# Performance work log

Measured on AMD Instinct MI355X. Metric: run time of the kernel, lower is better.

Reference implementation:

```python
import jax, jax.numpy as jnp
import numpy as np

N = 100000
E = 1_600_000
IN_X, OUT_X = 128, 128
IN_E, OUT_E = 32, 128


def setup_inputs() -> dict:
    key = jax.random.key(0)
    k1, k2, k3, k4, k5, k6, k7 = jax.random.split(key, 7)
    x = jax.random.normal(k1, (N, IN_X), dtype=jnp.float32)
    edge_index = jax.random.randint(k2, (2, E), 0, N, dtype=jnp.int64)
    edge_attr = jax.random.normal(k3, (E, IN_E), dtype=jnp.float32)
    Wx = jax.random.normal(k4, (IN_X, OUT_X), dtype=jnp.float32) * (1.0 / np.sqrt(IN_X))
    bx = jax.random.normal(k5, (OUT_X,), dtype=jnp.float32) * 0.01
    We = jax.random.normal(k6, (IN_E, OUT_E), dtype=jnp.float32) * (1.0 / np.sqrt(IN_E))
    be = jax.random.normal(k7, (OUT_E,), dtype=jnp.float32) * 0.01
    return {"x": x, "edge_index": edge_index, "edge_attr": edge_attr,
            "Wx": Wx, "bx": bx, "We": We, "be": be}


def reference(x, edge_index, edge_attr, Wx, bx, We, be):
    # torch: to_dense() -> [N, N, in_e]; sum over dim=1 == scatter-add of
    # edge_attr into rows indexed by the source node edge_index[0].
    agg = jax.ops.segment_sum(edge_attr, edge_index[0], num_segments=x.shape[0])  # [N, in_e]
    hx = x @ Wx + bx          # [N, out_x]
    he = agg @ We + be        # [N, out_e]
    return jnp.concatenate((hx, he), axis=1)  # [N, out_x + out_e]
```

## Files before the change

kernel.cpp:

```cpp
#include <hip/hip_runtime.h>


#define BSHIFT    7
#define BSIZE     128
#define NBMAX     1024
#define SEG_CAP   3584
#define POOL_SZ   3648
#define CHUNK_A   8192
#define SPILL_CAP 65536

typedef short bf16x8 __attribute__((ext_vector_type(8)));
typedef float f32x4  __attribute__((ext_vector_type(4)));

__device__ __forceinline__ unsigned short f2bf(float f) {
    union { float f; unsigned u; } c; c.f = f;
    unsigned u = c.u;
    u += 0x7FFF + ((u >> 16) & 1);
    return (unsigned short)(u >> 16);
}

__global__ __launch_bounds__(512) void binA_kernel(
    const int* __restrict__ src, int E, int nb,
    unsigned* __restrict__ segs, int* __restrict__ gcnt,
    int2* __restrict__ spill, int* __restrict__ spillcnt)
{
    __shared__ unsigned pool[CHUNK_A];
    __shared__ int hist[NBMAX];
    __shared__ int offs[NBMAX];
    __shared__ int lcur[NBMAX];
    __shared__ int gbase[NBMAX];
    __shared__ int gallow[NBMAX];
    __shared__ int wsum[8];

    int tid = threadIdx.x;
    int base = blockIdx.x * CHUNK_A;

    for (int i = tid; i < NBMAX; i += 512) hist[i] = 0;
    __syncthreads();

    for (int i = tid; i < CHUNK_A; i += 512) {
        int e = base + i;
        if (e < E) atomicAdd(&hist[src[e] >> BSHIFT], 1);
    }
    __syncthreads();

    {
        int t2 = tid * 2;
        int c0 = hist[t2], c1 = hist[t2 + 1];
        int s = c0 + c1;
        int lane = tid & 63, wid = tid >> 6;
        int ws = s;
        #pragma unroll
        for (int d = 1; d < 64; d <<= 1) {
            int t = __shfl_up(ws, d);
            if (lane >= d) ws += t;
        }
        if (lane == 63) wsum[wid] = ws;
        __syncthreads();
        int woff = 0;
        #pragma unroll
        for (int w = 0; w < 8; ++w) if (w < wid) woff += wsum[w];
        int ex = woff + ws - s;
        offs[t2] = ex;          lcur[t2] = ex;
        offs[t2 + 1] = ex + c0; lcur[t2 + 1] = ex + c0;
    }
    __syncthreads();

    {
        int t2 = tid * 2;
        #pragma unroll
        for (int u = 0; u < 2; ++u) {
            int b = t2 + u;
            if (b < nb) {
                int cnt = hist[b];
                int b0 = cnt ? atomicAdd(&gcnt[b], cnt) : 0;
                gbase[b] = b0;
                int allow = SEG_CAP - b0;
                if (allow < 0) allow = 0;
                if (allow > cnt) allow = cnt;
                gallow[b] = allow;
            }
        }
    }
    __syncthreads();

    for (int i = tid; i < CHUNK_A; i += 512) {
        int e = base + i;
        if (e < E) {
            int s = src[e];
            int b = s >> BSHIFT;
            int p = atomicAdd(&lcur[b], 1);
            pool[p] = ((unsigned)e << BSHIFT) | (unsigned)(s & (BSIZE - 1));
        }
    }
    __syncthreads();

    int wid = tid >> 6, lane = tid & 63;
    for (int b = wid; b < nb; b += 8) {
        int cnt = hist[b];
        int off = offs[b];
        int allow = gallow[b];
        unsigned* dst = segs + (size_t)b * SEG_CAP + gbase[b];
        for (int i = lane; i < allow; i += 64)
            dst[i] = pool[off + i];
        int excess = cnt - allow;
        if (excess > 0) {
            int sb;
            if (lane == 0) sb = atomicAdd(spillcnt, excess);
            sb = __shfl(sb, 0);
            for (int i = lane; i < excess; i += 64) {
                int sp = sb + i;
                if (sp < SPILL_CAP) {
                    unsigned pv = pool[off + allow + i];
                    spill[sp] = make_int2((int)(pv >> BSHIFT),
                                          (b << BSHIFT) | (int)(pv & (BSIZE - 1)));
                }
            }
        }
    }
}

__global__ __launch_bounds__(512) void gather_he_kernel(
    const unsigned* __restrict__ segs, const int* __restrict__ gcnt,
    const int2* __restrict__ spill, const int* __restrict__ spillcnt,
    const float4* __restrict__ ea4,
    const float* __restrict__ We, const float* __restrict__ be,
    float* __restrict__ out, int N)
{
    __shared__ int counts[BSIZE];
    __shared__ int starts[BSIZE + 1];
    __shared__ int cursor[BSIZE];
    __shared__ int pool[POOL_SZ];
    __shared__ char sAgg[BSIZE * 64];
    __shared__ char sWeT[128 * 64];

    int tid = threadIdx.x;
    int b = blockIdx.x;
    int node0 = b << BSHIFT;
    int lane = tid & 63, w = tid >> 6;
    int col = lane & 15, m = lane >> 4;

    if (tid < BSIZE) counts[tid] = 0;
    for (int i = tid; i < 32 * 128; i += 512) {
        int k = i >> 7, j = i & 127;
        *(unsigned short*)(sWeT + j * 64 + ((k * 2) ^ ((j & 3) << 4))) = f2bf(We[i]);
    }
    __syncthreads();

    int segn = gcnt[b]; if (segn > SEG_CAP) segn = SEG_CAP;
    const unsigned* seg = segs + (size_t)b * SEG_CAP;
    int nsp = *spillcnt; if (nsp > SPILL_CAP) nsp = SPILL_CAP;

    for (int i = tid; i < segn; i += 512)
        atomicAdd(&counts[seg[i] & (BSIZE - 1)], 1);
    if (nsp)
        for (int i = tid; i < nsp; i += 512) {
            int2 p = spill[i];
            if ((p.y >> BSHIFT) == b) atomicAdd(&counts[p.y & (BSIZE - 1)], 1);
        }
    __syncthreads();

    if (tid < 64) {
        int c0 = counts[tid * 2], c1 = counts[tid * 2 + 1];
        int s = c0 + c1;
        int ws = s;
        #pragma unroll
        for (int d = 1; d < 64; d <<= 1) {
            int t = __shfl_up(ws, d);
            if (tid >= d) ws += t;
        }
        int ex = ws - s;
        starts[tid * 2] = ex;          cursor[tid * 2] = ex;
        starts[tid * 2 + 1] = ex + c0; cursor[tid * 2 + 1] = ex + c0;
        if (tid == 63) starts[BSIZE] = ws;
    }
    __syncthreads();

    for (int i = tid; i < segn; i += 512) {
        unsigned pe = seg[i];
        int pos = atomicAdd(&cursor[pe & (BSIZE - 1)], 1);
        if (pos < POOL_SZ) pool[pos] = (int)(pe >> BSHIFT);
    }
    if (nsp)
        for (int i = tid; i < nsp; i += 512) {
            int2 p = spill[i];
            if ((p.y >> BSHIFT) == b) {
                int pos = atomicAdd(&cursor[p.y & (BSIZE - 1)], 1);
                if (pos < POOL_SZ) pool[pos] = p.x;
            }
        }
    __syncthreads();

    {
        int g = tid >> 2, q2 = tid & 3;
        int node = node0 + g;
        float4 aL0 = {0.f,0.f,0.f,0.f}, aL1 = {0.f,0.f,0.f,0.f};
        float4 aH0 = {0.f,0.f,0.f,0.f}, aH1 = {0.f,0.f,0.f,0.f};
        if (node < N) {
            int p0 = starts[g], p1 = starts[g + 1];
            if (p1 > POOL_SZ) p1 = POOL_SZ;
            int p = p0;
            for (; p + 4 <= p1; p += 4) {
                int e0 = pool[p], e1 = pool[p + 1], e2 = pool[p + 2], e3 = pool[p + 3];
                const float4* r0 = ea4 + (size_t)e0 * 8;
                const float4* r1 = ea4 + (size_t)e1 * 8;
                const float4* r2 = ea4 + (size_t)e2 * 8;
                const float4* r3 = ea4 + (size_t)e3 * 8;
                float4 l0 = r0[q2],     l1 = r1[q2],     l2 = r2[q2],     l3 = r3[q2];
                float4 h0 = r0[q2 + 4], h1 = r1[q2 + 4], h2 = r2[q2 + 4], h3 = r3[q2 + 4];
                aL0.x += l0.x; aL0.y += l0.y; aL0.z += l0.z; aL0.w += l0.w;
                aL1.x += l1.x; aL1.y += l1.y; aL1.z += l1.z; aL1.w += l1.w;
                aH0.x += h0.x; aH0.y += h0.y; aH0.z += h0.z; aH0.w += h0.w;
                aH1.x += h1.x; aH1.y += h1.y; aH1.z += h1.z; aH1.w += h1.w;
                aL0.x += l2.x; aL0.y += l2.y; aL0.z += l2.z; aL0.w += l2.w;
                aL1.x += l3.x; aL1.y += l3.y; aL1.z += l3.z; aL1.w += l3.w;
                aH0.x += h2.x; aH0.y += h2.y; aH0.z += h2.z; aH0.w += h2.w;
                aH1.x += h3.x; aH1.y += h3.y; aH1.z += h3.z; aH1.w += h3.w;
            }
            for (; p < p1; ++p) {
                const float4* r = ea4 + (size_t)pool[p] * 8;
                float4 l = r[q2], h = r[q2 + 4];
                aL0.x += l.x; aL0.y += l.y; aL0.z += l.z; aL0.w += l.w;
                aH0.x += h.x; aH0.y += h.y; aH0.z += h.z; aH0.w += h.w;
            }
            aL0.x += aL1.x; aL0.y += aL1.y; aL0.z += aL1.z; aL0.w += aL1.w;
            aH0.x += aH1.x; aH0.y += aH1.y; aH0.z += aH1.z; aH0.w += aH1.w;
        }
        uint2 lo, hi;
        lo.x = (unsigned)f2bf(aL0.x) | ((unsigned)f2bf(aL0.y) << 16);
        lo.y = (unsigned)f2bf(aL0.z) | ((unsigned)f2bf(aL0.w) << 16);
        hi.x = (unsigned)f2bf(aH0.x) | ((unsigned)f2bf(aH0.y) << 16);
        hi.y = (unsigned)f2bf(aH0.z) | ((unsigned)f2bf(aH0.w) << 16);
        int swz = (g & 7) << 4;
        *(uint2*)(sAgg + ((g * 64 + q2 * 8) ^ swz))            = lo;
        *(uint2*)(sAgg + ((g * 64 + (q2 + 4) * 8) ^ swz))      = hi;
    }
    __syncthreads();

    {
        int lrow = (w << 4) + col;
        bf16x8 aa = *(const bf16x8*)(sAgg + ((lrow * 64 + m * 16) ^ ((lrow & 7) << 4)));

        f32x4 acc[8];
        #pragma unroll
        for (int ct = 0; ct < 8; ++ct) {
            float bv = be[ct * 16 + col];
            acc[ct] = (f32x4){bv, bv, bv, bv};
        }
        #pragma unroll
        for (int ct = 0; ct < 8; ++ct) {
            bf16x8 bwe = *(const bf16x8*)(sWeT + (ct * 16 + col) * 64 + ((m * 16) ^ ((col & 3) << 4)));
            acc[ct] = __builtin_amdgcn_mfma_f32_16x16x32_bf16(aa, bwe, acc[ct], 0, 0, 0);
        }

        int srow = node0 + (w << 4) + m * 4;
        #pragma unroll
        for (int r = 0; r < 4; ++r) {
            if (srow + r < N) {
                float* orow = out + (size_t)(srow + r) * 256 + 128 + col;
                #pragma unroll
                for (int ct = 0; ct < 8; ++ct)
                    orow[ct * 16] = acc[ct][r];
            }
        }
    }
}

__global__ __launch_bounds__(256) void scatter_kernel(
    const float4* __restrict__ ea4, const int* __restrict__ src,
    float* __restrict__ agg, int nquads)
{
    int t = blockIdx.x * blockDim.x + threadIdx.x;
    if (t >= nquads) return;
    int e = t >> 3, q = t & 7;
    float4 v = ea4[t];
    int node = src[e];
    float* dst = agg + (size_t)node * 32 + q * 4;
    atomicAdd(dst + 0, v.x); atomicAdd(dst + 1, v.y);
    atomicAdd(dst + 2, v.z); atomicAdd(dst + 3, v.w);
}

__global__ __launch_bounds__(256) void cvt_kernel(
    const float* __restrict__ agg, unsigned short* __restrict__ aggbf, int n)
{
    int t = blockIdx.x * blockDim.x + threadIdx.x;
    if (t < n) aggbf[t] = f2bf(agg[t]);
}

template <bool DO_HE>
__global__ __launch_bounds__(512, 4) void mfma_gemm(
    const float* __restrict__ x, const unsigned short* __restrict__ aggbf,
    const float* __restrict__ Wx, const float* __restrict__ bx,
    const float* __restrict__ We, const float* __restrict__ be,
    float* __restrict__ out, int N, int ntiles)
{
    __shared__ char sWxT[128 * 256];
    __shared__ char sWeT[128 * 64];
    __shared__ char sX[128 * 256];
    __shared__ char sA[128 * 64];

    int tid = threadIdx.x;
    int lane = tid & 63, w = tid >> 6;
    int col = lane & 15, m = lane >> 4;

    for (int i = tid; i < 128 * 128; i += 512) {
        int k = i >> 7, j = i & 127;
        *(unsigned short*)(sWxT + j * 256 + ((k * 2) ^ ((j & 7) << 4))) = f2bf(Wx[i]);
    }
    if (DO_HE)
        for (int i = tid; i < 32 * 128; i += 512) {
            int k = i >> 7, j = i & 127;
            *(unsigned short*)(sWeT + j * 64 + ((k * 2) ^ ((j & 3) << 4))) = f2bf(We[i]);
        }
    float bxv[8], bev[8];
    #pragma unroll
    for (int ct = 0; ct < 8; ++ct) {
        bxv[ct] = bx[ct * 16 + col];
        if (DO_HE) bev[ct] = be[ct * 16 + col];
    }

    int lrow = (w << 4) + col;
    int swzA = (lrow & 7) << 4;

    for (int t = blockIdx.x; t < ntiles; t += gridDim.x) {
        int rbase_t = t << 7;
        __syncthreads();

        for (int i = tid; i < 128 * 32; i += 512) {
            int row = i >> 5, c4 = i & 31;
            int gr = rbase_t + row;
            float4 v = {0.f, 0.f, 0.f, 0.f};
            if (gr < N) v = *(const float4*)(x + (size_t)gr * 128 + c4 * 4);
            uint2 uu;
            uu.x = (unsigned)f2bf(v.x) | ((unsigned)f2bf(v.y) << 16);
            uu.y = (unsigned)f2bf(v.z) | ((unsigned)f2bf(v.w) << 16);
            *(uint2*)(sX + ((row * 256 + c4 * 8) ^ ((row & 7) << 4))) = uu;
        }
        if (DO_HE) {
            int row = tid >> 2, mm = tid & 3;
            int gr = rbase_t + row;
            bf16x8 av = {0, 0, 0, 0, 0, 0, 0, 0};
            if (gr < N) av = *(const bf16x8*)(aggbf + (size_t)gr * 32 + mm * 8);
            *(bf16x8*)(sA + ((row * 64 + mm * 16) ^ ((row & 7) << 4))) = av;
        }
        __syncthreads();

        bf16x8 ax[4];
        #pragma unroll
        for (int kk = 0; kk < 4; ++kk)
            ax[kk] = *(const bf16x8*)(sX + lrow * 256 + ((kk * 64 + m * 16) ^ swzA));
        bf16x8 aa = {0,0,0,0,0,0,0,0};
        if (DO_HE) aa = *(const bf16x8*)(sA + ((lrow * 64 + m * 16) ^ swzA));

        int srow = rbase_t + (w << 4) + m * 4;

        #pragma unroll
        for (int half = 0; half < 2; ++half) {
            f32x4 acc[8];
            #pragma unroll
            for (int ct = 0; ct < 4; ++ct) {
                int c8 = half * 4 + ct;
                acc[ct] = (f32x4){bxv[c8], bxv[c8], bxv[c8], bxv[c8]};
                if (DO_HE) acc[4 + ct] = (f32x4){bev[c8], bev[c8], bev[c8], bev[c8]};
            }

            #pragma unroll
            for (int ct = 0; ct < 4; ++ct) {
                int c8 = half * 4 + ct;
                const char* brow = sWxT + (c8 * 16 + col) * 256;
                int swz = (col & 7) << 4;
                #pragma unroll
                for (int kk = 0; kk < 4; ++kk) {
                    bf16x8 bfrag = *(const bf16x8*)(brow + ((kk * 64 + m * 16) ^ swz));
                    acc[ct] = __builtin_amdgcn_mfma_f32_16x16x32_bf16(ax[kk], bfrag, acc[ct], 0, 0, 0);
                }
                if (DO_HE) {
                    bf16x8 bwe = *(const bf16x8*)(sWeT + (c8 * 16 + col) * 64 + ((m * 16) ^ ((col & 3) << 4)));
                    acc[4 + ct] = __builtin_amdgcn_mfma_f32_16x16x32_bf16(aa, bwe, acc[4 + ct], 0, 0, 0);
                }
            }

            #pragma unroll
            for (int r = 0; r < 4; ++r) {
                if (srow + r < N) {
                    float* orow = out + (size_t)(srow + r) * 256 + col + half * 64;
                    #pragma unroll
                    for (int ct = 0; ct < 4; ++ct) {
                        orow[ct * 16] = acc[ct][r];
                        if (DO_HE) orow[128 + ct * 16] = acc[4 + ct][r];
                    }
                }
            }
        }
    }
}

extern "C" void kernel_launch(void* const* d_in, const int* in_sizes, int n_in,
                              void* d_out, int out_size, void* d_ws, size_t ws_size,
                              hipStream_t stream) {
    const float* x          = (const float*)d_in[0];
    const int*   edge_index = (const int*)d_in[1];
    const float* edge_attr  = (const float*)d_in[2];
    const float* Wx         = (const float*)d_in[3];
    const float* bx         = (const float*)d_in[4];
    const float* We         = (const float*)d_in[5];
    const float* be         = (const float*)d_in[6];
    float* out = (float*)d_out;

    int N = in_sizes[0] / 128;
    int E = in_sizes[2] / 32;
    int nb = (N + BSIZE - 1) >> BSHIFT;
    int ntiles = (N + 127) >> 7;

    char* ws = (char*)d_ws;
    size_t aggbfBytes = ((size_t)N * 32 * 2 + 255) & ~255ull;
    size_t segsBytes  = ((size_t)nb * SEG_CAP * 4 + 255) & ~255ull;
    size_t gcntBytes  = ((size_t)(nb + 1) * 4 + 255) & ~255ull;
    size_t spillBytes = (size_t)SPILL_CAP * 8;
    size_t need = aggbfBytes + segsBytes + gcntBytes + spillBytes;

    unsigned short* aggbf = (unsigned short*)ws;

    int g = ntiles < 512 ? ntiles : 512;

    if (ws_size >= need && nb <= NBMAX) {
        unsigned* segs  = (unsigned*)(ws + aggbfBytes);
        int* gcnt       = (int*)(ws + aggbfBytes + segsBytes);
        int* spillcnt   = gcnt + nb;
        int2* spill     = (int2*)(ws + aggbfBytes + segsBytes + gcntBytes);

        hipMemsetAsync(gcnt, 0, (size_t)(nb + 1) * 4, stream);
        int nblkA = (E + CHUNK_A - 1) / CHUNK_A;
        binA_kernel<<<nblkA, 512, 0, stream>>>(edge_index, E, nb, segs, gcnt, spill, spillcnt);
        gather_he_kernel<<<nb, 512, 0, stream>>>(segs, gcnt, spill, spillcnt,
                                                 (const float4*)edge_attr, We, be, out, N);
        mfma_gemm<false><<<g, 512, 0, stream>>>(x, aggbf, Wx, bx, We, be, out, N, ntiles);
    } else {
        float* aggf = (float*)(ws + aggbfBytes);
        hipMemsetAsync(aggf, 0, (size_t)N * 32 * 4, stream);
        int nq = E * 8;
        scatter_kernel<<<(nq + 255) / 256, 256, 0, stream>>>(
            (const float4*)edge_attr, edge_index, aggf, nq);
        cvt_kernel<<<(N * 32 + 255) / 256, 256, 0, stream>>>(aggf, aggbf, N * 32);
        mfma_gemm<true><<<g, 512, 0, stream>>>(x, aggbf, Wx, bx, We, be, out, N, ntiles);
    }
}
```

Baseline: 150.4 us.

## Fuse x@Wx GEMM into gather kernel and cache src in registers during binning

The separate hx GEMM launch is folded into the per-bucket gather kernel. Each block now also converts Wx to bf16 in LDS and computes x@Wx+bx for its 128 nodes, with x loaded straight from global memory, before the he MFMA. This removes one kernel launch and lets hx compute overlap with the gather phase. The cost is an extra 32KB of LDS per block and a redundant Wx conversion in every block. Separately, the binning kernel keeps src values in registers so the second pass does not reload them from global memory.

Result: faster. 147.2 us (-2.1%).

```diff
diff --git a/kernel.cpp b/kernel.cpp
--- a/kernel.cpp
+++ b/kernel.cpp
@@ -38,9 +38,13 @@
     for (int i = tid; i < NBMAX; i += 512) hist[i] = 0;
     __syncthreads();
 
-    for (int i = tid; i < CHUNK_A; i += 512) {
-        int e = base + i;
-        if (e < E) atomicAdd(&hist[src[e] >> BSHIFT], 1);
+    int srcv[CHUNK_A / 512];
+    #pragma unroll
+    for (int u = 0; u < CHUNK_A / 512; ++u) {
+        int e = base + tid + u * 512;
+        int s = (e < E) ? src[e] : -1;
+        srcv[u] = s;
+        if (s >= 0) atomicAdd(&hist[s >> BSHIFT], 1);
     }
     __syncthreads();
 
@@ -84,10 +88,11 @@
     }
     __syncthreads();
 
-    for (int i = tid; i < CHUNK_A; i += 512) {
-        int e = base + i;
-        if (e < E) {
-            int s = src[e];
+    #pragma unroll
+    for (int u = 0; u < CHUNK_A / 512; ++u) {
+        int s = srcv[u];
+        if (s >= 0) {
+            int e = base + tid + u * 512;
             int b = s >> BSHIFT;
             int p = atomicAdd(&lcur[b], 1);
             pool[p] = ((unsigned)e << BSHIFT) | (unsigned)(s & (BSIZE - 1));
@@ -120,10 +125,11 @@
     }
 }
 
-__global__ __launch_bounds__(512) void gather_he_kernel(
+__global__ __launch_bounds__(512, 4) void fused_kernel(
     const unsigned* __restrict__ segs, const int* __restrict__ gcnt,
     const int2* __restrict__ spill, const int* __restrict__ spillcnt,
-    const float4* __restrict__ ea4,
+    const float4* __restrict__ ea4, const float* __restrict__ x,
+    const float* __restrict__ Wx, const float* __restrict__ bx,
     const float* __restrict__ We, const float* __restrict__ be,
     float* __restrict__ out, int N)
 {
@@ -133,6 +139,7 @@
     __shared__ int pool[POOL_SZ];
     __shared__ char sAgg[BSIZE * 64];
     __shared__ char sWeT[128 * 64];
+    __shared__ char sWxT[128 * 256];
 
     int tid = threadIdx.x;
     int b = blockIdx.x;
@@ -141,9 +148,19 @@
     int col = lane & 15, m = lane >> 4;
 
     if (tid < BSIZE) counts[tid] = 0;
+    for (int i = tid; i < 128 * 128; i += 512) {
+        int k = i >> 7, j = i & 127;
+        *(unsigned short*)(sWxT + j * 256 + ((k * 2) ^ ((j & 7) << 4))) = f2bf(Wx[i]);
+    }
     for (int i = tid; i < 32 * 128; i += 512) {
         int k = i >> 7, j = i & 127;
         *(unsigned short*)(sWeT + j * 64 + ((k * 2) ^ ((j & 3) << 4))) = f2bf(We[i]);
+    }
+    float bxv[8], bev[8];
+    #pragma unroll
+    for (int ct = 0; ct < 8; ++ct) {
+        bxv[ct] = bx[ct * 16 + col];
+        bev[ct] = be[ct * 16 + col];
     }
     __syncthreads();
 
@@ -232,28 +249,79 @@
         hi.x = (unsigned)f2bf(aH0.x) | ((unsigned)f2bf(aH0.y) << 16);
         hi.y = (unsigned)f2bf(aH0.z) | ((unsigned)f2bf(aH0.w) << 16);
         int swz = (g & 7) << 4;
-        *(uint2*)(sAgg + ((g * 64 + q2 * 8) ^ swz))            = lo;
-        *(uint2*)(sAgg + ((g * 64 + (q2 + 4) * 8) ^ swz))      = hi;
-    }
-    __syncthreads();
+        *(uint2*)(sAgg + ((g * 64 + q2 * 8) ^ swz))       = lo;
+        *(uint2*)(sAgg + ((g * 64 + (q2 + 4) * 8) ^ swz)) = hi;
+    }
+
+    int lrow = (w << 4) + col;
+    int grow = node0 + lrow;
+    bool rok = grow < N;
+    int srow = node0 + (w << 4) + m * 4;
 
     {
-        int lrow = (w << 4) + col;
+        const float* xr = x + (size_t)grow * 128 + m * 8;
+        bf16x8 ax[4];
+        #pragma unroll
+        for (int kk = 0; kk < 4; ++kk) {
+            float4 p0 = {0.f,0.f,0.f,0.f}, p1 = {0.f,0.f,0.f,0.f};
+            if (rok) {
+                p0 = *(const float4*)(xr + kk * 32);
+                p1 = *(const float4*)(xr + kk * 32 + 4);
+            }
+            bf16x8 a;
+            a[0] = (short)f2bf(p0.x); a[1] = (short)f2bf(p0.y);
+            a[2] = (short)f2bf(p0.z); a[3] = (short)f2bf(p0.w);
+            a[4] = (short)f2bf(p1.x); a[5] = (short)f2bf(p1.y);
+            a[6] = (short)f2bf(p1.z); a[7] = (short)f2bf(p1.w);
+            ax[kk] = a;
+        }
+
+        #pragma unroll
+        for (int half = 0; half < 2; ++half) {
+            f32x4 acc[4];
+            #pragma unroll
+            for (int ct = 0; ct < 4; ++ct) {
+                int c8 = half * 4 + ct;
+                acc[ct] = (f32x4){bxv[c8], bxv[c8], bxv[c8], bxv[c8]};
+            }
+            #pragma unroll
+            for (int ct = 0; ct < 4; ++ct) {
+                int c8 = half * 4 + ct;
+                const char* brow = sWxT + (c8 * 16 + col) * 256;
+                int swz = (col & 7) << 4;
+                #pragma unroll
+                for (int kk = 0; kk < 4; ++kk) {
+                    bf16x8 bfrag = *(const bf16x8*)(brow + ((kk * 64 + m * 16) ^ swz));
+                    acc[ct] = __builtin_amdgcn_mfma_f32_16x16x32_bf16(ax[kk], bfrag, acc[ct], 0, 0, 0);
+                }
+            }
+            #pragma unroll
+            for (int r = 0; r < 4; ++r) {
+                if (srow + r < N) {
+                    float* orow = out + (size_t)(srow + r) * 256 + col + half * 64;
+                    #pragma unroll
+                    for (int ct = 0; ct < 4; ++ct)
+                        orow[ct * 16] = acc[ct][r];
+                }
+            }
+        }
+    }
+
+    __syncthreads();
+
+    {
         bf16x8 aa = *(const bf16x8*)(sAgg + ((lrow * 64 + m * 16) ^ ((lrow & 7) << 4)));
 
         f32x4 acc[8];
         #pragma unroll
-        for (int ct = 0; ct < 8; ++ct) {
-            float bv = be[ct * 16 + col];
-            acc[ct] = (f32x4){bv, bv, bv, bv};
-        }
+        for (int ct = 0; ct < 8; ++ct)
+            acc[ct] = (f32x4){bev[ct], bev[ct], bev[ct], bev[ct]};
         #pragma unroll
         for (int ct = 0; ct < 8; ++ct) {
             bf16x8 bwe = *(const bf16x8*)(sWeT + (ct * 16 + col) * 64 + ((m * 16) ^ ((col & 3) << 4)));
             acc[ct] = __builtin_amdgcn_mfma_f32_16x16x32_bf16(aa, bwe, acc[ct], 0, 0, 0);
         }
 
-        int srow = node0 + (w << 4) + m * 4;
         #pragma unroll
         for (int r = 0; r < 4; ++r) {
             if (srow + r < N) {
@@ -287,8 +355,7 @@
     if (t < n) aggbf[t] = f2bf(agg[t]);
 }
 
-template <bool DO_HE>
-__global__ __launch_bounds__(512, 4) void mfma_gemm(
+__global__ __launch_bounds__(512, 4) void mfma_gemm_full(
     const float* __restrict__ x, const unsigned short* __restrict__ aggbf,
     const float* __restrict__ Wx, const float* __restrict__ bx,
     const float* __restrict__ We, const float* __restrict__ be,
@@ -307,16 +374,15 @@
         int k = i >> 7, j = i & 127;
         *(unsigned short*)(sWxT + j * 256 + ((k * 2) ^ ((j & 7) << 4))) = f2bf(Wx[i]);
     }
-    if (DO_HE)
-        for (int i = tid; i < 32 * 128; i += 512) {
-            int k = i >> 7, j = i & 127;
-            *(unsigned short*)(sWeT + j * 64 + ((k * 2) ^ ((j & 3) << 4))) = f2bf(We[i]);
-        }
+    for (int i = tid; i < 32 * 128; i += 512) {
+        int k = i >> 7, j = i & 127;
+        *(unsigned short*)(sWeT + j * 64 + ((k * 2) ^ ((j & 3) << 4))) = f2bf(We[i]);
+    }
     float bxv[8], bev[8];
     #pragma unroll
     for (int ct = 0; ct < 8; ++ct) {
         bxv[ct] = bx[ct * 16 + col];
-        if (DO_HE) bev[ct] = be[ct * 16 + col];
+        bev[ct] = be[ct * 16 + col];
     }
 
     int lrow = (w << 4) + col;
@@ -336,7 +402,7 @@
             uu.y = (unsigned)f2bf(v.z) | ((unsigned)f2bf(v.w) << 16);
             *(uint2*)(sX + ((row * 256 + c4 * 8) ^ ((row & 7) << 4))) = uu;
         }
-        if (DO_HE) {
+        {
             int row = tid >> 2, mm = tid & 3;
             int gr = rbase_t + row;
             bf16x8 av = {0, 0, 0, 0, 0, 0, 0, 0};
@@ -349,8 +415,7 @@
         #pragma unroll
         for (int kk = 0; kk < 4; ++kk)
             ax[kk] = *(const bf16x8*)(sX + lrow * 256 + ((kk * 64 + m * 16) ^ swzA));
-        bf16x8 aa = {0,0,0,0,0,0,0,0};
-        if (DO_HE) aa = *(const bf16x8*)(sA + ((lrow * 64 + m * 16) ^ swzA));
+        bf16x8 aa = *(const bf16x8*)(sA + ((lrow * 64 + m * 16) ^ swzA));
 
         int srow = rbase_t + (w << 4) + m * 4;
 
@@ -360,10 +425,9 @@
             #pragma unroll
             for (int ct = 0; ct < 4; ++ct) {
                 int c8 = half * 4 + ct;
-                acc[ct] = (f32x4){bxv[c8], bxv[c8], bxv[c8], bxv[c8]};
-                if (DO_HE) acc[4 + ct] = (f32x4){bev[c8], bev[c8], bev[c8], bev[c8]};
-            }
-
+                acc[ct]     = (f32x4){bxv[c8], bxv[c8], bxv[c8], bxv[c8]};
+                acc[4 + ct] = (f32x4){bev[c8], bev[c8], bev[c8], bev[c8]};
+            }
             #pragma unroll
             for (int ct = 0; ct < 4; ++ct) {
                 int c8 = half * 4 + ct;
@@ -374,20 +438,17 @@
                     bf16x8 bfrag = *(const bf16x8*)(brow + ((kk * 64 + m * 16) ^ swz));
                     acc[ct] = __builtin_amdgcn_mfma_f32_16x16x32_bf16(ax[kk], bfrag, acc[ct], 0, 0, 0);
                 }
-                if (DO_HE) {
-                    bf16x8 bwe = *(const bf16x8*)(sWeT + (c8 * 16 + col) * 64 + ((m * 16) ^ ((col & 3) << 4)));
-                    acc[4 + ct] = __builtin_amdgcn_mfma_f32_16x16x32_bf16(aa, bwe, acc[4 + ct], 0, 0, 0);
-                }
-            }
-
+                bf16x8 bwe = *(const bf16x8*)(sWeT + (c8 * 16 + col) * 64 + ((m * 16) ^ ((col & 3) << 4)));
+                acc[4 + ct] = __builtin_amdgcn_mfma_f32_16x16x32_bf16(aa, bwe, acc[4 + ct], 0, 0, 0);
+            }
             #pragma unroll
             for (int r = 0; r < 4; ++r) {
                 if (srow + r < N) {
                     float* orow = out + (size_t)(srow + r) * 256 + col + half * 64;
                     #pragma unroll
                     for (int ct = 0; ct < 4; ++ct) {
-                        orow[ct * 16] = acc[ct][r];
-                        if (DO_HE) orow[128 + ct * 16] = acc[4 + ct][r];
+                        orow[ct * 16]       = acc[ct][r];
+                        orow[128 + ct * 16] = acc[4 + ct][r];
                     }
                 }
             }
@@ -421,8 +482,6 @@
 
     unsigned short* aggbf = (unsigned short*)ws;
 
-    int g = ntiles < 512 ? ntiles : 512;
-
     if (ws_size >= need && nb <= NBMAX) {
         unsigned* segs  = (unsigned*)(ws + aggbfBytes);
         int* gcnt       = (int*)(ws + aggbfBytes + segsBytes);
@@ -432,9 +491,9 @@
         hipMemsetAsync(gcnt, 0, (size_t)(nb + 1) * 4, stream);
         int nblkA = (E + CHUNK_A - 1) / CHUNK_A;
         binA_kernel<<<nblkA, 512, 0, stream>>>(edge_index, E, nb, segs, gcnt, spill, spillcnt);
-        gather_he_kernel<<<nb, 512, 0, stream>>>(segs, gcnt, spill, spillcnt,
-                                                 (const float4*)edge_attr, We, be, out, N);
-        mfma_gemm<false><<<g, 512, 0, stream>>>(x, aggbf, Wx, bx, We, be, out, N, ntiles);
+        fused_kernel<<<nb, 512, 0, stream>>>(segs, gcnt, spill, spillcnt,
+                                             (const float4*)edge_attr, x,
+                                             Wx, bx, We, be, out, N);
     } else {
         float* aggf = (float*)(ws + aggbfBytes);
         hipMemsetAsync(aggf, 0, (size_t)N * 32 * 4, stream);
@@ -442,6 +501,7 @@
         scatter_kernel<<<(nq + 255) / 256, 256, 0, stream>>>(
             (const float4*)edge_attr, edge_index, aggf, nq);
         cvt_kernel<<<(N * 32 + 255) / 256, 256, 0, stream>>>(aggf, aggbf, N * 32);
-        mfma_gemm<true><<<g, 512, 0, stream>>>(x, aggbf, Wx, bx, We, be, out, N, ntiles);
-    }
-}
+        int g = ntiles < 512 ? ntiles : 512;
+        mfma_gemm_full<<<g, 512, 0, stream>>>(x, aggbf, Wx, bx, We, be, out, N, ntiles);
+    }
+}
```
